# Kernel optimization log

Measured on AMD Instinct MI355X. Metric: run time of the kernel, lower is better.

## Reference

```python
import jax, jax.numpy as jnp
import numpy as np

N = 50000
E = 800000
IN_DIM = 128
HID = 128
OUT = 128
HEADS = 4
HD_HID = HID // HEADS   # 32
HD_OUT = OUT // HEADS   # 32
NEG_SLOPE = 0.2


def gat_layer(H, src, dst, W, a_src, a_dst, b, num_nodes):
    """Standard GAT layer with concatenated heads.
    H: [N, Fin]; W: [Fin, heads*hd]; a_src/a_dst: [heads, hd]; b: [heads*hd]."""
    heads, hd = a_src.shape
    h = (H @ W).reshape(num_nodes, heads, hd)            # [N, H, D]
    alpha_s = jnp.einsum('nhd,hd->nh', h, a_src)         # [N, H]
    alpha_d = jnp.einsum('nhd,hd->nh', h, a_dst)         # [N, H]
    logits = alpha_s[src] + alpha_d[dst]                 # [E, H]
    logits = jax.nn.leaky_relu(logits, NEG_SLOPE)
    # segment softmax over incoming edges of each destination node
    seg_max = jax.ops.segment_max(logits, dst, num_segments=num_nodes)
    seg_max = jnp.where(jnp.isfinite(seg_max), seg_max, 0.0)
    ex = jnp.exp(logits - seg_max[dst])                  # [E, H]
    denom = jax.ops.segment_sum(ex, dst, num_segments=num_nodes)  # [N, H]
    att = ex / jnp.maximum(denom, 1e-16)[dst]            # [E, H]
    msg = att[:, :, None] * h[src]                       # [E, H, D]
    out = jax.ops.segment_sum(msg, dst, num_segments=num_nodes)   # [N, H, D]
    return out.reshape(num_nodes, heads * hd) + b


def setup_inputs() -> dict:
    key = jax.random.key(0)
    ks = jax.random.split(key, 10)
    X_all = jax.random.normal(ks[0], (N, IN_DIM), dtype=jnp.float32)
    edge_index = jax.random.randint(ks[1], (2, E), 0, N, dtype=jnp.int64)
    s0 = 1.0 / np.sqrt(IN_DIM)
    s1 = 1.0 / np.sqrt(HID)
    W0 = jax.random.normal(ks[2], (IN_DIM, HEADS * HD_HID), dtype=jnp.float32) * s0
    a_src0 = jax.random.normal(ks[3], (HEADS, HD_HID), dtype=jnp.float32) * s1
    a_dst0 = jax.random.normal(ks[4], (HEADS, HD_HID), dtype=jnp.float32) * s1
    b0 = jnp.zeros((HEADS * HD_HID,), dtype=jnp.float32)
    W1 = jax.random.normal(ks[5], (HID, HEADS * HD_OUT), dtype=jnp.float32) * s1
    a_src1 = jax.random.normal(ks[6], (HEADS, HD_OUT), dtype=jnp.float32) * s1
    a_dst1 = jax.random.normal(ks[7], (HEADS, HD_OUT), dtype=jnp.float32) * s1
    b1 = jnp.zeros((HEADS * HD_OUT,), dtype=jnp.float32)
    return {"X_all": X_all, "edge_index": edge_index,
            "W0": W0, "a_src0": a_src0, "a_dst0": a_dst0, "b0": b0,
            "W1": W1, "a_src1": a_src1, "a_dst1": a_dst1, "b1": b1}


def reference(X_all, edge_index, W0, a_src0, a_dst0, b0, W1, a_src1, a_dst1, b1):
    src, dst = edge_index[0], edge_index[1]
    num_nodes = X_all.shape[0]
    # layer 1 + ELU (dropout is identity in eval mode)
    H = gat_layer(X_all, src, dst, W0, a_src0, a_dst0, b0, num_nodes)
    H = jax.nn.elu(H)
    # layer 2 + ELU
    H = gat_layer(H, src, dst, W1, a_src1, a_dst1, b1, num_nodes)
    H = jax.nn.elu(H)
    return H
```

## Files before the change

### kernel.cpp

```cpp
#include <hip/hip_runtime.h>
#include <math.h>
#include <float.h>

#define NNODES 50000
#define NEDGES 800000

#define KB    196
#define NPB   256
#define CAPB  4608
#define EPB   4096
#define NABLK ((NEDGES + EPB - 1) / EPB)

typedef __attribute__((ext_vector_type(4))) _Float16 half4;
typedef __attribute__((ext_vector_type(8))) _Float16 half8;

__global__ __launch_bounds__(256) void bininit_kernel(int* __restrict__ bincur) {
    int t = threadIdx.x;
    if (t < KB) bincur[t] = t * CAPB;
}

__global__ __launch_bounds__(256) void binA_kernel(
    const int* __restrict__ src, const int* __restrict__ dst,
    int* __restrict__ bincur, unsigned* __restrict__ binned)
{
    __shared__ int lhist[KB];
    __shared__ int lstart[KB];
    __shared__ int lcur[KB];
    __shared__ int gbase[KB];
    __shared__ unsigned lbuf[EPB];
    __shared__ int wtot[4];

    int t = threadIdx.x;
    int e0 = blockIdx.x * EPB;
    int ecnt = NEDGES - e0; if (ecnt > EPB) ecnt = EPB;

    for (int b = t; b < KB; b += 256) lhist[b] = 0;
    __syncthreads();

    for (int idx = t; idx < ecnt; idx += 256)
        atomicAdd(&lhist[((unsigned)dst[e0 + idx]) >> 8], 1);
    __syncthreads();

    {
        int lane = t & 63, w = t >> 6;
        int v = (t < KB) ? lhist[t] : 0;
        int x = v;
#pragma unroll
        for (int off = 1; off < 64; off <<= 1) {
            int y = __shfl_up(x, off, 64);
            if (lane >= off) x += y;
        }
        if (lane == 63) wtot[w] = x;
        __syncthreads();
        int wpre = 0;
#pragma unroll
        for (int j = 0; j < 4; ++j) if (j < w) wpre += wtot[j];
        int ex = wpre + x - v;
        if (t < KB) { lstart[t] = ex; lcur[t] = ex; }
    }
    __syncthreads();

    if (t < KB) {
        int c = lhist[t];
        gbase[t] = c ? atomicAdd(&bincur[t], c) : 0;
    }
    __syncthreads();

    for (int idx = t; idx < ecnt; idx += 256) {
        unsigned d = (unsigned)dst[e0 + idx];
        unsigned s = (unsigned)src[e0 + idx];
        int pos = atomicAdd(&lcur[d >> 8], 1);
        lbuf[pos] = (d << 16) | s;
    }
    __syncthreads();

    for (int idx = t; idx < ecnt; idx += 256) {
        unsigned p = lbuf[idx];
        int b = p >> 24;
        binned[gbase[b] + (idx - lstart[b])] = p;
    }
}

__global__ __launch_bounds__(256) void binB_kernel(
    const unsigned* __restrict__ binned, const int* __restrict__ bincur,
    int* __restrict__ csr_src, int2* __restrict__ node_info)
{
    __shared__ int lhist[NPB];
    __shared__ int lcur[NPB];
    __shared__ int wtot[4];
    int k = blockIdx.x;
    int t = threadIdx.x;
    int base = k * CAPB;
    int cnt = bincur[k] - base;

    lhist[t] = 0;
    __syncthreads();

    for (int i = t; i < cnt; i += 256)
        atomicAdd(&lhist[(binned[base + i] >> 16) & 0xFF], 1);
    __syncthreads();

    int lane = t & 63, w = t >> 6;
    int v = lhist[t];
    int x = v;
#pragma unroll
    for (int off = 1; off < 64; off <<= 1) {
        int y = __shfl_up(x, off, 64);
        if (lane >= off) x += y;
    }
    if (lane == 63) wtot[w] = x;
    __syncthreads();
    int wpre = 0;
#pragma unroll
    for (int j = 0; j < 4; ++j) if (j < w) wpre += wtot[j];
    int ex = wpre + x - v;
    lcur[t] = ex;
    int node = k * NPB + t;
    if (node < NNODES) node_info[node] = make_int2(base + ex, v);
    __syncthreads();

    for (int i = t; i < cnt; i += 256) {
        unsigned p = binned[base + i];
        int ln = (p >> 16) & 0xFF;
        int pos = atomicAdd(&lcur[ln], 1);
        csr_src[base + pos] = (int)(p & 0xFFFFu);
    }
}

#define GBM 128
#define GBK 32
__global__ __launch_bounds__(256) void gemm_alpha_kernel(
    const float* __restrict__ X, const float* __restrict__ W,
    const float* __restrict__ avs, const float* __restrict__ avd,
    _Float16* __restrict__ Hh, float* __restrict__ alpha_s, float* __restrict__ alpha_d,
    int nrows)
{
    __shared__ float Xs[GBK][GBM];
    __shared__ float Ws[GBK][128];

    int t = threadIdx.x;
    int row0 = (t >> 4) * 8;
    int col0 = (t & 15) * 8;
    int block_row = blockIdx.x * GBM;

    float acc[8][8];
#pragma unroll
    for (int i = 0; i < 8; ++i)
#pragma unroll
        for (int j = 0; j < 8; ++j) acc[i][j] = 0.f;

    for (int k0 = 0; k0 < 128; k0 += GBK) {
        {
            int r  = t >> 1;
            int kb = (t & 1) * 16;
            int grow = block_row + r;
            float4 v0 = make_float4(0,0,0,0), v1 = v0, v2 = v0, v3 = v0;
            if (grow < nrows) {
                const float* p = X + (size_t)grow * 128 + k0 + kb;
                v0 = ((const float4*)p)[0];
                v1 = ((const float4*)p)[1];
                v2 = ((const float4*)p)[2];
                v3 = ((const float4*)p)[3];
            }
            Xs[kb+ 0][r] = v0.x; Xs[kb+ 1][r] = v0.y; Xs[kb+ 2][r] = v0.z; Xs[kb+ 3][r] = v0.w;
            Xs[kb+ 4][r] = v1.x; Xs[kb+ 5][r] = v1.y; Xs[kb+ 6][r] = v1.z; Xs[kb+ 7][r] = v1.w;
            Xs[kb+ 8][r] = v2.x; Xs[kb+ 9][r] = v2.y; Xs[kb+10][r] = v2.z; Xs[kb+11][r] = v2.w;
            Xs[kb+12][r] = v3.x; Xs[kb+13][r] = v3.y; Xs[kb+14][r] = v3.z; Xs[kb+15][r] = v3.w;
        }
        {
            int kr = t >> 3;
            int cc = (t & 7) * 16;
            const float* p = W + (size_t)(k0 + kr) * 128 + cc;
            float4 w0 = ((const float4*)p)[0];
            float4 w1 = ((const float4*)p)[1];
            float4 w2 = ((const float4*)p)[2];
            float4 w3 = ((const float4*)p)[3];
            *(float4*)&Ws[kr][cc + 0]  = w0;
            *(float4*)&Ws[kr][cc + 4]  = w1;
            *(float4*)&Ws[kr][cc + 8]  = w2;
            *(float4*)&Ws[kr][cc + 12] = w3;
        }
        __syncthreads();
#pragma unroll
        for (int kk = 0; kk < GBK; ++kk) {
            float4 a0 = *(const float4*)&Xs[kk][row0];
            float4 a1 = *(const float4*)&Xs[kk][row0 + 4];
            float4 w0 = *(const float4*)&Ws[kk][col0];
            float4 w1 = *(const float4*)&Ws[kk][col0 + 4];
            float av[8] = {a0.x, a0.y, a0.z, a0.w, a1.x, a1.y, a1.z, a1.w};
            float wv[8] = {w0.x, w0.y, w0.z, w0.w, w1.x, w1.y, w1.z, w1.w};
#pragma unroll
            for (int i = 0; i < 8; ++i)
#pragma unroll
                for (int j = 0; j < 8; ++j)
                    acc[i][j] = fmaf(av[i], wv[j], acc[i][j]);
        }
        __syncthreads();
    }

    int cg = t & 15;
    int head = cg >> 2;
    const float* asrc = avs + head * 32 + (cg & 3) * 8;
    const float* adst = avd + head * 32 + (cg & 3) * 8;
#pragma unroll
    for (int i = 0; i < 8; ++i) {
        int grow = block_row + row0 + i;
        bool ok = (grow < nrows);
        if (ok) {
            half8 hv;
#pragma unroll
            for (int j = 0; j < 8; ++j) hv[j] = (_Float16)acc[i][j];
            *(half8*)&Hh[(size_t)grow * 128 + col0] = hv;
        }
        float ps = 0.f, pd = 0.f;
#pragma unroll
        for (int j = 0; j < 8; ++j) {
            ps = fmaf(acc[i][j], asrc[j], ps);
            pd = fmaf(acc[i][j], adst[j], pd);
        }
        ps += __shfl_xor(ps, 1); ps += __shfl_xor(ps, 2);
        pd += __shfl_xor(pd, 1); pd += __shfl_xor(pd, 2);
        if (ok && (cg & 3) == 0) {
            alpha_s[grow * 4 + head] = ps;
            alpha_d[grow * 4 + head] = pd;
        }
    }
}

__global__ __launch_bounds__(256) void att_gather_kernel(
    const int* __restrict__ csr_src, const int2* __restrict__ node_info,
    const float* __restrict__ alpha_s, const float* __restrict__ alpha_d,
    const _Float16* __restrict__ hbuf, const float* __restrict__ b,
    float* __restrict__ out)
{
    int node = blockIdx.x * 4 + (threadIdx.x >> 6);
    if (node >= NNODES) return;
    int lane = threadIdx.x & 63;
    int half = lane >> 5;
    int q    = lane & 31;
    int f    = q * 4;
    int hh   = q >> 3;
    int2 bi = node_info[node];
    int beg = bi.x, end = bi.x + bi.y;
    float ad = alpha_d[node * 4 + hh];

    float4 a4 = make_float4(0.f, 0.f, 0.f, 0.f);
    float den = 0.f;
    int i = beg + half;
    for (; i + 6 < end; i += 8) {
        int s0 = csr_src[i];
        int s1 = csr_src[i + 2];
        int s2 = csr_src[i + 4];
        int s3 = csr_src[i + 6];
        float l0 = alpha_s[s0 * 4 + hh] + ad;
        float l1 = alpha_s[s1 * 4 + hh] + ad;
        float l2 = alpha_s[s2 * 4 + hh] + ad;
        float l3 = alpha_s[s3 * 4 + hh] + ad;
        half4 h0 = *(const half4*)(hbuf + (size_t)s0 * 128 + f);
        half4 h1 = *(const half4*)(hbuf + (size_t)s1 * 128 + f);
        half4 h2 = *(const half4*)(hbuf + (size_t)s2 * 128 + f);
        half4 h3 = *(const half4*)(hbuf + (size_t)s3 * 128 + f);
        l0 = (l0 >= 0.f) ? l0 : 0.2f * l0;
        l1 = (l1 >= 0.f) ? l1 : 0.2f * l1;
        l2 = (l2 >= 0.f) ? l2 : 0.2f * l2;
        l3 = (l3 >= 0.f) ? l3 : 0.2f * l3;
        float e0 = __expf(l0);
        float e1 = __expf(l1);
        float e2 = __expf(l2);
        float e3 = __expf(l3);
        den += (e0 + e1) + (e2 + e3);
        a4.x = fmaf(e0, (float)h0[0], a4.x); a4.y = fmaf(e0, (float)h0[1], a4.y);
        a4.z = fmaf(e0, (float)h0[2], a4.z); a4.w = fmaf(e0, (float)h0[3], a4.w);
        a4.x = fmaf(e1, (float)h1[0], a4.x); a4.y = fmaf(e1, (float)h1[1], a4.y);
        a4.z = fmaf(e1, (float)h1[2], a4.z); a4.w = fmaf(e1, (float)h1[3], a4.w);
        a4.x = fmaf(e2, (float)h2[0], a4.x); a4.y = fmaf(e2, (float)h2[1], a4.y);
        a4.z = fmaf(e2, (float)h2[2], a4.z); a4.w = fmaf(e2, (float)h2[3], a4.w);
        a4.x = fmaf(e3, (float)h3[0], a4.x); a4.y = fmaf(e3, (float)h3[1], a4.y);
        a4.z = fmaf(e3, (float)h3[2], a4.z); a4.w = fmaf(e3, (float)h3[3], a4.w);
    }
    for (; i < end; i += 2) {
        int s0 = csr_src[i];
        float l0 = alpha_s[s0 * 4 + hh] + ad;
        l0 = (l0 >= 0.f) ? l0 : 0.2f * l0;
        float e0 = __expf(l0);
        half4 h0 = *(const half4*)(hbuf + (size_t)s0 * 128 + f);
        den += e0;
        a4.x = fmaf(e0, (float)h0[0], a4.x); a4.y = fmaf(e0, (float)h0[1], a4.y);
        a4.z = fmaf(e0, (float)h0[2], a4.z); a4.w = fmaf(e0, (float)h0[3], a4.w);
    }

    a4.x += __shfl_xor(a4.x, 32);
    a4.y += __shfl_xor(a4.y, 32);
    a4.z += __shfl_xor(a4.z, 32);
    a4.w += __shfl_xor(a4.w, 32);
    den  += __shfl_xor(den, 32);

    if (half == 0) {
        float rd = 1.f / fmaxf(den, 1e-16f);
        float4 bv = *(const float4*)(b + f);
        float x0 = a4.x * rd + bv.x;
        float x1 = a4.y * rd + bv.y;
        float x2 = a4.z * rd + bv.z;
        float x3 = a4.w * rd + bv.w;
        x0 = (x0 > 0.f) ? x0 : expm1f(x0);
        x1 = (x1 > 0.f) ? x1 : expm1f(x1);
        x2 = (x2 > 0.f) ? x2 : expm1f(x2);
        x3 = (x3 > 0.f) ? x3 : expm1f(x3);
        *(float4*)(out + (size_t)node * 128 + f) = make_float4(x0, x1, x2, x3);
    }
}

extern "C" void kernel_launch(void* const* d_in, const int* in_sizes, int n_in,
                              void* d_out, int out_size, void* d_ws, size_t ws_size,
                              hipStream_t stream) {
    const float* X    = (const float*)d_in[0];
    const int*   ei   = (const int*)d_in[1];
    const float* W0   = (const float*)d_in[2];
    const float* as0  = (const float*)d_in[3];
    const float* ad0  = (const float*)d_in[4];
    const float* b0   = (const float*)d_in[5];
    const float* W1   = (const float*)d_in[6];
    const float* as1  = (const float*)d_in[7];
    const float* ad1  = (const float*)d_in[8];
    const float* b1   = (const float*)d_in[9];

    const int* srcp = ei;
    const int* dstp = ei + NEDGES;

    float* ws = (float*)d_ws;
    _Float16* h16 = (_Float16*)ws;
    float* hout = ws + 3200000;
    float* as_  = hout + 6400000;
    float* ad_  = as_  + 200000;
    unsigned* binned = (unsigned*)(ad_ + 200000);
    int*  csr_src   = (int*)(binned + (KB + 1) * CAPB);
    int2* node_info = (int2*)(csr_src + KB * CAPB);
    int*  bincur    = (int*)(node_info + NNODES);

    bininit_kernel<<<1, 256, 0, stream>>>(bincur);
    binA_kernel<<<NABLK, 256, 0, stream>>>(srcp, dstp, bincur, binned);
    binB_kernel<<<KB, 256, 0, stream>>>(binned, bincur, csr_src, node_info);

    const int NODE_BLOCKS = (NNODES + 3) / 4;

    for (int layer = 0; layer < 2; ++layer) {
        const float* Hin = layer ? hout : X;
        const float* W   = layer ? W1  : W0;
        const float* avs = layer ? as1 : as0;
        const float* avd = layer ? ad1 : ad0;
        const float* bv  = layer ? b1  : b0;
        float* outp      = layer ? (float*)d_out : hout;

        gemm_alpha_kernel<<<(NNODES + GBM - 1) / GBM, 256, 0, stream>>>(
            Hin, W, avs, avd, h16, as_, ad_, NNODES);

        att_gather_kernel<<<NODE_BLOCKS, 256, 0, stream>>>(
            csr_src, node_info, as_, ad_, h16, bv, outp);
    }
}
```

Baseline: 173.2 us.

## Use fp16 MFMA GEMM and fp16 intermediate layer activations

Replaces the fp32 FMA-based GEMM with an MFMA 16x16x32 fp16 kernel. A new prep kernel converts X to fp16 and transposes and converts both weight matrices. The first layer's gather now writes its ELU output in fp16, so the second GEMM reads half the bytes. This cuts GEMM compute and memory traffic but adds a conversion pass over X and lowers input precision.

After: 160.2 us. 1.08x faster.

```diff
diff --git a/kernel.cpp b/kernel.cpp
--- a/kernel.cpp
+++ b/kernel.cpp
@@ -13,6 +13,7 @@
 
 typedef __attribute__((ext_vector_type(4))) _Float16 half4;
 typedef __attribute__((ext_vector_type(8))) _Float16 half8;
+typedef __attribute__((ext_vector_type(4))) float f32x4;
 
 __global__ __launch_bounds__(256) void bininit_kernel(int* __restrict__ bincur) {
     int t = threadIdx.x;
@@ -127,111 +128,119 @@
     }
 }
 
-#define GBM 128
-#define GBK 32
-__global__ __launch_bounds__(256) void gemm_alpha_kernel(
-    const float* __restrict__ X, const float* __restrict__ W,
+__global__ __launch_bounds__(256) void prep_kernel(
+    const float* __restrict__ X, const float* __restrict__ W0,
+    const float* __restrict__ W1, _Float16* __restrict__ X16,
+    _Float16* __restrict__ W0t, _Float16* __restrict__ W1t)
+{
+    int i = blockIdx.x * 256 + threadIdx.x;
+    int stride = gridDim.x * 256;
+    const int nx4 = NNODES * 128 / 4;
+    for (int idx = i; idx < nx4; idx += stride) {
+        float4 v = ((const float4*)X)[idx];
+        half4 h = {(_Float16)v.x, (_Float16)v.y, (_Float16)v.z, (_Float16)v.w};
+        ((half4*)X16)[idx] = h;
+    }
+    for (int idx = i; idx < 128 * 128; idx += stride) {
+        int cc = idx >> 7, k = idx & 127;
+        W0t[idx] = (_Float16)W0[k * 128 + cc];
+        W1t[idx] = (_Float16)W1[k * 128 + cc];
+    }
+}
+
+#define GP 136
+__global__ __launch_bounds__(256) void gemm_mfma_kernel(
+    const _Float16* __restrict__ A, const _Float16* __restrict__ Wt,
     const float* __restrict__ avs, const float* __restrict__ avd,
-    _Float16* __restrict__ Hh, float* __restrict__ alpha_s, float* __restrict__ alpha_d,
-    int nrows)
-{
-    __shared__ float Xs[GBK][GBM];
-    __shared__ float Ws[GBK][128];
+    _Float16* __restrict__ Hh, float* __restrict__ alpha_s,
+    float* __restrict__ alpha_d, int nrows)
+{
+    __shared__ _Float16 Xs[64 * GP];
+    __shared__ _Float16 Ws[128 * GP];
 
     int t = threadIdx.x;
-    int row0 = (t >> 4) * 8;
-    int col0 = (t & 15) * 8;
-    int block_row = blockIdx.x * GBM;
-
-    float acc[8][8];
-#pragma unroll
-    for (int i = 0; i < 8; ++i)
-#pragma unroll
-        for (int j = 0; j < 8; ++j) acc[i][j] = 0.f;
-
-    for (int k0 = 0; k0 < 128; k0 += GBK) {
-        {
-            int r  = t >> 1;
-            int kb = (t & 1) * 16;
-            int grow = block_row + r;
-            float4 v0 = make_float4(0,0,0,0), v1 = v0, v2 = v0, v3 = v0;
-            if (grow < nrows) {
-                const float* p = X + (size_t)grow * 128 + k0 + kb;
-                v0 = ((const float4*)p)[0];
-                v1 = ((const float4*)p)[1];
-                v2 = ((const float4*)p)[2];
-                v3 = ((const float4*)p)[3];
+    int brow = blockIdx.x * 64;
+
+    {
+        int r = t >> 2, q = t & 3;
+        int grow = brow + r;
+        half8 v0 = {}, v1 = {}, v2 = {}, v3 = {};
+        if (grow < nrows) {
+            const half8* p = (const half8*)(A + (size_t)grow * 128 + q * 32);
+            v0 = p[0]; v1 = p[1]; v2 = p[2]; v3 = p[3];
+        }
+        _Float16* d = Xs + r * GP + q * 32;
+        *(half8*)(d + 0)  = v0; *(half8*)(d + 8)  = v1;
+        *(half8*)(d + 16) = v2; *(half8*)(d + 24) = v3;
+    }
+    {
+        int wr = t >> 1, wh = t & 1;
+        const half8* p = (const half8*)(Wt + wr * 128 + wh * 64);
+        _Float16* d = Ws + wr * GP + wh * 64;
+#pragma unroll
+        for (int j = 0; j < 8; ++j) *(half8*)(d + j * 8) = p[j];
+    }
+    __syncthreads();
+
+    int wv = t >> 6, l = t & 63;
+    int lrow = l & 15;
+    int lk8  = (l >> 4) * 8;
+
+    f32x4 acc[8];
+#pragma unroll
+    for (int n = 0; n < 8; ++n) acc[n] = (f32x4){0.f, 0.f, 0.f, 0.f};
+
+    const _Float16* xbase = Xs + (wv * 16 + lrow) * GP + lk8;
+#pragma unroll
+    for (int kk = 0; kk < 4; ++kk) {
+        half8 a = *(const half8*)(xbase + kk * 32);
+#pragma unroll
+        for (int n = 0; n < 8; ++n) {
+            half8 bf = *(const half8*)(Ws + (n * 16 + lrow) * GP + kk * 32 + lk8);
+            acc[n] = __builtin_amdgcn_mfma_f32_16x16x32_f16(a, bf, acc[n], 0, 0, 0);
+        }
+    }
+
+    int c = lrow;
+    int g = l >> 4;
+#pragma unroll
+    for (int n = 0; n < 8; ++n) {
+#pragma unroll
+        for (int r = 0; r < 4; ++r) {
+            int row = brow + wv * 16 + g * 4 + r;
+            if (row < nrows)
+                Hh[(size_t)row * 128 + n * 16 + c] = (_Float16)acc[n][r];
+        }
+    }
+#pragma unroll
+    for (int hd = 0; hd < 4; ++hd) {
+        float as0 = avs[hd * 32 + c], as1 = avs[hd * 32 + 16 + c];
+        float ad0 = avd[hd * 32 + c], ad1 = avd[hd * 32 + 16 + c];
+#pragma unroll
+        for (int r = 0; r < 4; ++r) {
+            float ps = acc[2 * hd][r] * as0 + acc[2 * hd + 1][r] * as1;
+            float pd = acc[2 * hd][r] * ad0 + acc[2 * hd + 1][r] * ad1;
+            ps += __shfl_xor(ps, 1); ps += __shfl_xor(ps, 2);
+            ps += __shfl_xor(ps, 4); ps += __shfl_xor(ps, 8);
+            pd += __shfl_xor(pd, 1); pd += __shfl_xor(pd, 2);
+            pd += __shfl_xor(pd, 4); pd += __shfl_xor(pd, 8);
+            if (c == 0) {
+                int row = brow + wv * 16 + g * 4 + r;
+                if (row < nrows) {
+                    alpha_s[row * 4 + hd] = ps;
+                    alpha_d[row * 4 + hd] = pd;
+                }
             }
-            Xs[kb+ 0][r] = v0.x; Xs[kb+ 1][r] = v0.y; Xs[kb+ 2][r] = v0.z; Xs[kb+ 3][r] = v0.w;
-            Xs[kb+ 4][r] = v1.x; Xs[kb+ 5][r] = v1.y; Xs[kb+ 6][r] = v1.z; Xs[kb+ 7][r] = v1.w;
-            Xs[kb+ 8][r] = v2.x; Xs[kb+ 9][r] = v2.y; Xs[kb+10][r] = v2.z; Xs[kb+11][r] = v2.w;
-            Xs[kb+12][r] = v3.x; Xs[kb+13][r] = v3.y; Xs[kb+14][r] = v3.z; Xs[kb+15][r] = v3.w;
-        }
-        {
-            int kr = t >> 3;
-            int cc = (t & 7) * 16;
-            const float* p = W + (size_t)(k0 + kr) * 128 + cc;
-            float4 w0 = ((const float4*)p)[0];
-            float4 w1 = ((const float4*)p)[1];
-            float4 w2 = ((const float4*)p)[2];
-            float4 w3 = ((const float4*)p)[3];
-            *(float4*)&Ws[kr][cc + 0]  = w0;
-            *(float4*)&Ws[kr][cc + 4]  = w1;
-            *(float4*)&Ws[kr][cc + 8]  = w2;
-            *(float4*)&Ws[kr][cc + 12] = w3;
-        }
-        __syncthreads();
-#pragma unroll
-        for (int kk = 0; kk < GBK; ++kk) {
-            float4 a0 = *(const float4*)&Xs[kk][row0];
-            float4 a1 = *(const float4*)&Xs[kk][row0 + 4];
-            float4 w0 = *(const float4*)&Ws[kk][col0];
-            float4 w1 = *(const float4*)&Ws[kk][col0 + 4];
-            float av[8] = {a0.x, a0.y, a0.z, a0.w, a1.x, a1.y, a1.z, a1.w};
-            float wv[8] = {w0.x, w0.y, w0.z, w0.w, w1.x, w1.y, w1.z, w1.w};
-#pragma unroll
-            for (int i = 0; i < 8; ++i)
-#pragma unroll
-                for (int j = 0; j < 8; ++j)
-                    acc[i][j] = fmaf(av[i], wv[j], acc[i][j]);
-        }
-        __syncthreads();
-    }
-
-    int cg = t & 15;
-    int head = cg >> 2;
-    const float* asrc = avs + head * 32 + (cg & 3) * 8;
-    const float* adst = avd + head * 32 + (cg & 3) * 8;
-#pragma unroll
-    for (int i = 0; i < 8; ++i) {
-        int grow = block_row + row0 + i;
-        bool ok = (grow < nrows);
-        if (ok) {
-            half8 hv;
-#pragma unroll
-            for (int j = 0; j < 8; ++j) hv[j] = (_Float16)acc[i][j];
-            *(half8*)&Hh[(size_t)grow * 128 + col0] = hv;
-        }
-        float ps = 0.f, pd = 0.f;
-#pragma unroll
-        for (int j = 0; j < 8; ++j) {
-            ps = fmaf(acc[i][j], asrc[j], ps);
-            pd = fmaf(acc[i][j], adst[j], pd);
-        }
-        ps += __shfl_xor(ps, 1); ps += __shfl_xor(ps, 2);
-        pd += __shfl_xor(pd, 1); pd += __shfl_xor(pd, 2);
-        if (ok && (cg & 3) == 0) {
-            alpha_s[grow * 4 + head] = ps;
-            alpha_d[grow * 4 + head] = pd;
-        }
-    }
-}
-
+        }
+    }
+}
+
+template <bool F16OUT>
 __global__ __launch_bounds__(256) void att_gather_kernel(
     const int* __restrict__ csr_src, const int2* __restrict__ node_info,
     const float* __restrict__ alpha_s, const float* __restrict__ alpha_d,
     const _Float16* __restrict__ hbuf, const float* __restrict__ b,
-    float* __restrict__ out)
+    float* __restrict__ out32, _Float16* __restrict__ out16)
 {
     int node = blockIdx.x * 4 + (threadIdx.x >> 6);
     if (node >= NNODES) return;
@@ -306,7 +315,12 @@
         x1 = (x1 > 0.f) ? x1 : expm1f(x1);
         x2 = (x2 > 0.f) ? x2 : expm1f(x2);
         x3 = (x3 > 0.f) ? x3 : expm1f(x3);
-        *(float4*)(out + (size_t)node * 128 + f) = make_float4(x0, x1, x2, x3);
+        if (F16OUT) {
+            half4 hv = {(_Float16)x0, (_Float16)x1, (_Float16)x2, (_Float16)x3};
+            *(half4*)(out16 + (size_t)node * 128 + f) = hv;
+        } else {
+            *(float4*)(out32 + (size_t)node * 128 + f) = make_float4(x0, x1, x2, x3);
+        }
     }
 }
 
@@ -327,11 +341,13 @@
     const int* srcp = ei;
     const int* dstp = ei + NEDGES;
 
-    float* ws = (float*)d_ws;
-    _Float16* h16 = (_Float16*)ws;
-    float* hout = ws + 3200000;
-    float* as_  = hout + 6400000;
-    float* ad_  = as_  + 200000;
+    _Float16* X16  = (_Float16*)d_ws;
+    _Float16* h16  = X16 + 6400000;
+    _Float16* ho16 = h16 + 6400000;
+    _Float16* W0t  = ho16 + 6400000;
+    _Float16* W1t  = W0t + 16384;
+    float* as_ = (float*)(W1t + 16384);
+    float* ad_ = as_ + 200000;
     unsigned* binned = (unsigned*)(ad_ + 200000);
     int*  csr_src   = (int*)(binned + (KB + 1) * CAPB);
     int2* node_info = (int2*)(csr_src + KB * CAPB);
@@ -341,20 +357,18 @@
     binA_kernel<<<NABLK, 256, 0, stream>>>(srcp, dstp, bincur, binned);
     binB_kernel<<<KB, 256, 0, stream>>>(binned, bincur, csr_src, node_info);
 
+    prep_kernel<<<2048, 256, 0, stream>>>(X, W0, W1, X16, W0t, W1t);
+
     const int NODE_BLOCKS = (NNODES + 3) / 4;
-
-    for (int layer = 0; layer < 2; ++layer) {
-        const float* Hin = layer ? hout : X;
-        const float* W   = layer ? W1  : W0;
-        const float* avs = layer ? as1 : as0;
-        const float* avd = layer ? ad1 : ad0;
-        const float* bv  = layer ? b1  : b0;
-        float* outp      = layer ? (float*)d_out : hout;
-
-        gemm_alpha_kernel<<<(NNODES + GBM - 1) / GBM, 256, 0, stream>>>(
-            Hin, W, avs, avd, h16, as_, ad_, NNODES);
-
-        att_gather_kernel<<<NODE_BLOCKS, 256, 0, stream>>>(
-            csr_src, node_info, as_, ad_, h16, bv, outp);
-    }
-}
+    const int GEMM_BLOCKS = (NNODES + 63) / 64;
+
+    gemm_mfma_kernel<<<GEMM_BLOCKS, 256, 0, stream>>>(
+        X16, W0t, as0, ad0, h16, as_, ad_, NNODES);
+    att_gather_kernel<true><<<NODE_BLOCKS, 256, 0, stream>>>(
+        csr_src, node_info, as_, ad_, h16, b0, nullptr, ho16);
+
+    gemm_mfma_kernel<<<GEMM_BLOCKS, 256, 0, stream>>>(
+        ho16, W1t, as1, ad1, h16, as_, ad_, NNODES);
+    att_gather_kernel<false><<<NODE_BLOCKS, 256, 0, stream>>>(
+        csr_src, node_info, as_, ad_, h16, b1, (float*)d_out, nullptr);
+}
```
